# Optimization experiments

Measured on AMD Instinct MI355X. Metric: run time of the kernel, lower is better.

The kernel has to match this reference:

```python
import jax, jax.numpy as jnp
import numpy as np

# shapes
B, S, D, V = 2, 2048, 1024, 32000
C = 8            # n_cycles
P = 256          # actual planes = min(n_planes_init, D // 2)
EPS = 1.1920929e-07  # torch RMSNorm default eps for float32 (finfo.eps)


def _rmsnorm(x, w):
    ms = jnp.mean(x * x, axis=-1, keepdims=True)
    return x * jax.lax.rsqrt(ms + EPS) * w


def setup_inputs() -> dict:
    key = jax.random.key(0)
    ks = jax.random.split(key, 10)
    tokens = jax.random.randint(ks[0], (B, S), 0, V, dtype=jnp.int32)
    embed_weight = jax.random.normal(ks[1], (V, D), dtype=jnp.float32) * 0.02
    lm_head_weight = jax.random.normal(ks[2], (V, D), dtype=jnp.float32) * 0.02
    out_norm_weight = jnp.ones((D,), dtype=jnp.float32)
    # per-cycle learned params (non-trivial values for numerics)
    angles = jax.random.normal(ks[3], (C, P), dtype=jnp.float32) * 0.1
    scales = 1.0 + jax.random.normal(ks[4], (C, D), dtype=jnp.float32) * 0.01
    shifts = jax.random.normal(ks[5], (C, D), dtype=jnp.float32) * 0.01
    norm_weights = 1.0 + jax.random.normal(ks[6], (C, D), dtype=jnp.float32) * 0.01
    mix_weight = jnp.array([0.1, 0.8, 0.1], dtype=jnp.float32)
    # plane pairs: per-cycle permutation of D, pi = perm[:P], pj = perm[P:2P]
    pi_list, pj_list = [], []
    for c in range(C):
        perm = jax.random.permutation(jax.random.fold_in(ks[7], c), D)
        pi_list.append(perm[:P])
        pj_list.append(perm[P:2 * P])
    pi_all = jnp.stack(pi_list).astype(jnp.int32)  # [C, P]
    pj_all = jnp.stack(pj_list).astype(jnp.int32)  # [C, P]
    return {
        "tokens": tokens,
        "embed_weight": embed_weight,
        "angles": angles,
        "scales": scales,
        "shifts": shifts,
        "norm_weights": norm_weights,
        "mix_weight": mix_weight,
        "out_norm_weight": out_norm_weight,
        "lm_head_weight": lm_head_weight,
        "pi_all": pi_all,
        "pj_all": pj_all,
    }


def reference(tokens, embed_weight, angles, scales, shifts, norm_weights,
              mix_weight, out_norm_weight, lm_head_weight, pi_all, pj_all):
    x = embed_weight[tokens].astype(jnp.float32)  # [B, S, D]
    n_cycles = angles.shape[0]
    for c in range(n_cycles):
        # temporal mix: shifted-left / self / shifted-right
        left = jnp.pad(x[:, :-1, :], ((0, 0), (1, 0), (0, 0)))
        right = jnp.pad(x[:, 1:, :], ((0, 0), (0, 1), (0, 0)))
        x = mix_weight[0] * left + mix_weight[1] * x + mix_weight[2] * right
        # Givens rotations on disjoint plane pairs (gather -> rotate -> scatter)
        pi, pj = pi_all[c], pj_all[c]
        cos_a = jnp.cos(angles[c])
        sin_a = jnp.sin(angles[c])
        xi = x[..., pi]  # [B, S, P]
        xj = x[..., pj]
        x_new = x.at[..., pi].set(xi * cos_a - xj * sin_a)
        x_new = x_new.at[..., pj].set(xi * sin_a + xj * cos_a)
        # scale/shift + SiLU, then RMSNorm residual update
        x_act = jax.nn.silu(x_new * scales[c] + shifts[c])
        x = x + _rmsnorm(x_act - x, norm_weights[c])
    x = _rmsnorm(x, out_norm_weight)
    return jnp.einsum("bsd,vd->bsv", x, lm_head_weight)  # [B, S, V]
```

## Files before the change

kernel.cpp:

```cpp
#include <hip/hip_runtime.h>

#define B_SZ   2
#define S_LEN  2048
#define D_DIM  1024
#define V_DIM  32000
#define NTOK   (B_SZ * S_LEN)
#define NCYC   8
#define NPLANES 256
#define EPS_F  1.1920929e-07f
#define NTILE  2000

typedef float  f32x4  __attribute__((ext_vector_type(4)));
typedef __bf16 bf16x8 __attribute__((ext_vector_type(8)));

__device__ __forceinline__ unsigned short f32_to_bf16(float f) {
    unsigned int u = __builtin_bit_cast(unsigned int, f);
    u += 0x7fffu + ((u >> 16) & 1u);
    return (unsigned short)(u >> 16);
}

__global__ __launch_bounds__(512, 2) void k_chain(
    const int* __restrict__ tokens, const float* __restrict__ table,
    const float* __restrict__ angles, const float* __restrict__ scales,
    const float* __restrict__ shifts, const float* __restrict__ normw,
    const float* __restrict__ mixw, const float* __restrict__ outnw,
    const int* __restrict__ pi_all, const int* __restrict__ pj_all,
    const float* __restrict__ lmhead,
    unsigned short* __restrict__ xbf, unsigned short* __restrict__ wbf)
{
    __shared__ float lx[32][D_DIM];
    __shared__ float red[8][32];
    const int blk = blockIdx.x, tid = threadIdx.x;
    const int wv = tid >> 6, ln = tid & 63;
    const int t0 = blk << 4;
    const int s0 = t0 & (S_LEN - 1);
    const int seqbase = t0 & ~(S_LEN - 1);
    const int c2 = tid << 1;

    const float mw0 = mixw[0], mw1 = mixw[1], mw2 = mixw[2];

    unsigned int svmask = 0;
    #pragma unroll
    for (int r = 0; r < 32; ++r) {
        const int s = s0 - 8 + r;
        const bool sv = (s >= 0) && (s < S_LEN);
        if (sv) svmask |= (1u << r);
        float2 v = make_float2(0.f, 0.f);
        if (sv) {
            const int tok = tokens[seqbase + s];
            v = *(const float2*)(table + (size_t)tok * D_DIM + c2);
        }
        lx[r][c2] = v.x; lx[r][c2 + 1] = v.y;
    }
    __syncthreads();

    float2 mreg[31], rres[31];

    for (int c = 0; c < NCYC; ++c) {
        const float2 sc = *(const float2*)(scales + c * D_DIM + c2);
        const float2 sh = *(const float2*)(shifts + c * D_DIM + c2);
        const float2 nw = *(const float2*)(normw  + c * D_DIM + c2);
        const int p    = tid & 255;
        const int half = tid >> 8;
        const int ip = pi_all[c * NPLANES + p];
        const int jp = pj_all[c * NPLANES + p];
        float sa, ca;
        sincosf(angles[c * NPLANES + p], &sa, &ca);

        #pragma unroll
        for (int r = 1; r <= 30; ++r) {
            if (r >= c + 1 && r < 31 - c && ((svmask >> r) & 1)) {
                const float2 a = make_float2(lx[r - 1][c2], lx[r - 1][c2 + 1]);
                const float2 b = make_float2(lx[r][c2],     lx[r][c2 + 1]);
                const float2 d = make_float2(lx[r + 1][c2], lx[r + 1][c2 + 1]);
                mreg[r].x = mw0 * a.x + mw1 * b.x + mw2 * d.x;
                mreg[r].y = mw0 * a.y + mw1 * b.y + mw2 * d.y;
            }
        }
        __syncthreads();
        #pragma unroll
        for (int r = 1; r <= 30; ++r) {
            if (r >= c + 1 && r < 31 - c && ((svmask >> r) & 1)) {
                lx[r][c2] = mreg[r].x; lx[r][c2 + 1] = mreg[r].y;
            }
        }
        __syncthreads();
        #pragma unroll
        for (int r = 1; r <= 30; ++r) {
            if (r >= c + 1 && r < 31 - c && ((svmask >> r) & 1) && (r & 1) == half) {
                const float xi = lx[r][ip], xj = lx[r][jp];
                lx[r][ip] = xi * ca - xj * sa;
                lx[r][jp] = xi * sa + xj * ca;
            }
        }
        __syncthreads();
        #pragma unroll
        for (int r = 1; r <= 30; ++r) {
            if (r >= c + 1 && r < 31 - c && ((svmask >> r) & 1)) {
                const float v0 = lx[r][c2], v1 = lx[r][c2 + 1];
                const float a0 = v0 * sc.x + sh.x;
                const float a1 = v1 * sc.y + sh.y;
                rres[r].x = a0 / (1.f + expf(-a0)) - mreg[r].x;
                rres[r].y = a1 / (1.f + expf(-a1)) - mreg[r].y;
                float pp = rres[r].x * rres[r].x + rres[r].y * rres[r].y;
                #pragma unroll
                for (int off = 32; off > 0; off >>= 1)
                    pp += __shfl_down(pp, off, 64);
                if (ln == 0) red[wv][r] = pp;
            }
        }
        __syncthreads();
        #pragma unroll
        for (int r = 1; r <= 30; ++r) {
            if (r >= c + 1 && r < 31 - c && ((svmask >> r) & 1)) {
                const float tot = red[0][r] + red[1][r] + red[2][r] + red[3][r]
                                + red[4][r] + red[5][r] + red[6][r] + red[7][r];
                const float inv = rsqrtf(tot * (1.0f / D_DIM) + EPS_F);
                lx[r][c2]     = mreg[r].x + rres[r].x * inv * nw.x;
                lx[r][c2 + 1] = mreg[r].y + rres[r].y * inv * nw.y;
            }
        }
        __syncthreads();
    }

    const float2 ow = *(const float2*)(outnw + c2);
    #pragma unroll
    for (int r = 8; r < 24; ++r) {
        const float v0 = lx[r][c2], v1 = lx[r][c2 + 1];
        float pp = v0 * v0 + v1 * v1;
        #pragma unroll
        for (int off = 32; off > 0; off >>= 1)
            pp += __shfl_down(pp, off, 64);
        if (ln == 0) red[wv][r - 8] = pp;
    }
    __syncthreads();
    #pragma unroll
    for (int r = 8; r < 24; ++r) {
        const float tot = red[0][r - 8] + red[1][r - 8] + red[2][r - 8] + red[3][r - 8]
                        + red[4][r - 8] + red[5][r - 8] + red[6][r - 8] + red[7][r - 8];
        const float inv = rsqrtf(tot * (1.0f / D_DIM) + EPS_F);
        const float v0 = lx[r][c2], v1 = lx[r][c2 + 1];
        ushort2 o = make_ushort2(f32_to_bf16(v0 * inv * ow.x),
                                 f32_to_bf16(v1 * inv * ow.y));
        *(ushort2*)(xbf + (size_t)(t0 + r - 8) * D_DIM + c2) = o;
    }

    for (int i = blk * 512 + tid; i < (V_DIM * D_DIM) / 4; i += 256 * 512) {
        const float4 v = ((const float4*)lmhead)[i];
        const ushort4 o = make_ushort4(f32_to_bf16(v.x), f32_to_bf16(v.y),
                                       f32_to_bf16(v.z), f32_to_bf16(v.w));
        ((ushort4*)wbf)[i] = o;
    }
}

#define GLD_LDS(g, l)                                                          \
    __builtin_amdgcn_global_load_lds(                                          \
        (const __attribute__((address_space(1))) void*)(g),                    \
        (__attribute__((address_space(3))) void*)(l), 16, 0, 0)

#define STAGE_A(BUF, H, KT, P) do {                                            \
    GLD_LDS((P) + (size_t)(H) * 131072 + (size_t)(KT) * 64,                    \
            &lds[(BUF) * 32768 + (H) * 8192 + wave * 1024]);                   \
    GLD_LDS((P) + (size_t)(H) * 131072 + 8192 + (size_t)(KT) * 64,             \
            &lds[(BUF) * 32768 + (H) * 8192 + wave * 1024 + 512]);             \
} while (0)

#define STAGE_B(BUF, H, KT, P) do {                                            \
    GLD_LDS((P) + (size_t)(H) * 131072 + (size_t)(KT) * 64,                    \
            &lds[16384 + (BUF) * 32768 + (H) * 8192 + wave * 1024]);           \
    GLD_LDS((P) + (size_t)(H) * 131072 + 8192 + (size_t)(KT) * 64,             \
            &lds[16384 + (BUF) * 32768 + (H) * 8192 + wave * 1024 + 512]);     \
} while (0)

#define RD_A(BUF, MIB) do { _Pragma("unroll")                                  \
    for (int q_ = 0; q_ < 4; ++q_) {                                           \
        afr[q_][0] = *(const bf16x8*)&lds[(BUF) * 32768 + aoff + ((MIB) + q_) * 1024 + kx0]; \
        afr[q_][1] = *(const bf16x8*)&lds[(BUF) * 32768 + aoff + ((MIB) + q_) * 1024 + kx1]; \
    } } while (0)

#define RD_B(BUF, NIB, DST) do { _Pragma("unroll")                             \
    for (int n_ = 0; n_ < 2; ++n_) {                                           \
        DST[n_][0] = *(const bf16x8*)&lds[(BUF) * 32768 + boff + ((NIB) + n_) * 1024 + kx0]; \
        DST[n_][1] = *(const bf16x8*)&lds[(BUF) * 32768 + boff + ((NIB) + n_) * 1024 + kx1]; \
    } } while (0)

#define MFMA16(MIB, NIB, BF) do {                                              \
    __builtin_amdgcn_s_setprio(1);                                             \
    _Pragma("unroll") for (int m_ = 0; m_ < 4; ++m_)                           \
    _Pragma("unroll") for (int n_ = 0; n_ < 2; ++n_) {                         \
        acc[(MIB) + m_][(NIB) + n_] = __builtin_amdgcn_mfma_f32_16x16x32_bf16( \
            afr[m_][0], BF[n_][0], acc[(MIB) + m_][(NIB) + n_], 0, 0, 0);      \
        acc[(MIB) + m_][(NIB) + n_] = __builtin_amdgcn_mfma_f32_16x16x32_bf16( \
            afr[m_][1], BF[n_][1], acc[(MIB) + m_][(NIB) + n_], 0, 0, 0);      \
    }                                                                          \
    __builtin_amdgcn_s_setprio(0); } while (0)

#define PH_SYNC() do { __builtin_amdgcn_s_barrier();                           \
    asm volatile("s_waitcnt lgkmcnt(0)" ::: "memory"); } while (0)
#define PH_END() do { asm volatile("" ::: "memory");                           \
    __builtin_amdgcn_s_barrier(); } while (0)
#define VMCNT4() asm volatile("s_waitcnt vmcnt(4)" ::: "memory")

__global__ __launch_bounds__(512, 2) void k_gemm(
    const unsigned short* __restrict__ A,
    const unsigned short* __restrict__ Bw,
    float* __restrict__ C)
{
    __shared__ __align__(16) unsigned short lds[65536];
    const int tid = threadIdx.x;
    const int wave = tid >> 6, lane = tid & 63;
    const int wm = wave >> 2, wn = wave & 3;
    const int lr = lane & 15, kg = lane >> 4;

    const int xr  = (lane & 7) * 8;
    const int kx0 = (kg * 8) ^ xr;
    const int kx1 = (32 + kg * 8) ^ xr;
    const int aoff = (wm * 128 + lr) * 64;
    const int boff = 16384 + (wn * 64 + lr) * 64;

    const int srow = lane >> 3;
    const int scol = ((lane & 7) ^ srow) * 8;
    const int soff = (wave * 16 + srow) * 1024 + scol;

    const int xcd = blockIdx.x & 7;
    const int rr  = blockIdx.x >> 3;
    const int tbase = xcd * 250 + rr * 8;
    const int ntile_mine = (rr == 31) ? 2 : 8;

    int T  = tbase;
    int bm = T & 15, bn = T >> 4;
    const unsigned short* gA = A  + (size_t)(bm * 256) * 1024 + soff;
    const unsigned short* gB = Bw + (size_t)(bn * 256) * 1024 + soff;

    bf16x8 afr[4][2], b01[2][2], b23[2][2];

    STAGE_A(0, 0, 0, gA); STAGE_A(0, 1, 0, gA);
    STAGE_B(0, 0, 0, gB); STAGE_B(0, 1, 0, gB);
    STAGE_B(1, 0, 1, gB); STAGE_B(1, 1, 1, gB);
    VMCNT4();
    __builtin_amdgcn_s_barrier();

    for (int t = 0; t < ntile_mine; ++t) {
        const bool last = (t == ntile_mine - 1);
        const int Tn = last ? T : T + 1;
        const int bm2 = Tn & 15, bn2 = Tn >> 4;
        const unsigned short* gA2 = A  + (size_t)(bm2 * 256) * 1024 + soff;
        const unsigned short* gB2 = Bw + (size_t)(bn2 * 256) * 1024 + soff;

        f32x4 acc[8][4];
        #pragma unroll
        for (int i = 0; i < 8; ++i)
            #pragma unroll
            for (int j2 = 0; j2 < 4; ++j2) acc[i][j2] = (f32x4){0.f, 0.f, 0.f, 0.f};

        for (int j = 0; j < 8; ++j) {
            const unsigned short* sA = (j == 7) ? gA2 : gA;
            const unsigned short* sB = (j == 7) ? gB2 : gB;
            const int k1 = 2 * j + 1;
            const int k2 = (2 * j + 2) & 15;
            const int k3 = (2 * j + 3) & 15;

            RD_A(0, 0); RD_B(0, 0, b01);
            STAGE_A(1, 0, k1, gA);
            PH_SYNC(); MFMA16(0, 0, b01); PH_END();

            RD_B(0, 2, b23);
            STAGE_A(1, 1, k1, gA);
            PH_SYNC(); MFMA16(0, 2, b23); PH_END();

            RD_A(0, 4);
            STAGE_B(0, 0, k2, sB);
            PH_SYNC(); MFMA16(4, 2, b23); PH_END();

            STAGE_B(0, 1, k2, sB);
            VMCNT4();
            PH_SYNC(); MFMA16(4, 0, b01); PH_END();

            RD_A(1, 0); RD_B(1, 0, b01);
            STAGE_A(0, 0, k2, sA);
            PH_SYNC(); MFMA16(0, 0, b01); PH_END();

            RD_B(1, 2, b23);
            STAGE_A(0, 1, k2, sA);
            PH_SYNC(); MFMA16(0, 2, b23); PH_END();

            RD_A(1, 4);
            STAGE_B(1, 0, k3, sB);
            PH_SYNC(); MFMA16(4, 2, b23); PH_END();

            STAGE_B(1, 1, k3, sB);
            VMCNT4();
            PH_SYNC(); MFMA16(4, 0, b01); PH_END();
        }

        #pragma unroll
        for (int mi = 0; mi < 8; ++mi) {
            const size_t m0 = (size_t)(bm * 256 + wm * 128 + mi * 16 + kg * 4);
            #pragma unroll
            for (int ni = 0; ni < 4; ++ni) {
                const int n = bn * 256 + wn * 64 + ni * 16 + lr;
                float* cp = C + m0 * V_DIM + n;
                cp[0]                 = acc[mi][ni][0];
                cp[(size_t)V_DIM]     = acc[mi][ni][1];
                cp[(size_t)2 * V_DIM] = acc[mi][ni][2];
                cp[(size_t)3 * V_DIM] = acc[mi][ni][3];
            }
        }

        T = Tn; bm = bm2; bn = bn2; gA = gA2; gB = gB2;
    }
}

extern "C" void kernel_launch(void* const* d_in, const int* in_sizes, int n_in,
                              void* d_out, int out_size, void* d_ws, size_t ws_size,
                              hipStream_t stream)
{
    const int*   tokens = (const int*)  d_in[0];
    const float* embedw = (const float*)d_in[1];
    const float* angles = (const float*)d_in[2];
    const float* scales = (const float*)d_in[3];
    const float* shifts = (const float*)d_in[4];
    const float* normw  = (const float*)d_in[5];
    const float* mixw   = (const float*)d_in[6];
    const float* outnw  = (const float*)d_in[7];
    const float* lmhead = (const float*)d_in[8];
    const int*   pi_all = (const int*)  d_in[9];
    const int*   pj_all = (const int*)  d_in[10];
    float* out = (float*)d_out;

    unsigned short* xbf = (unsigned short*)d_ws;
    unsigned short* wbf = xbf + (size_t)NTOK * D_DIM;

    k_chain<<<NTOK / 16, 512, 0, stream>>>(tokens, embedw, angles, scales,
        shifts, normw, mixw, outnw, pi_all, pj_all, lmhead, xbf, wbf);

    k_gemm<<<256, 512, 0, stream>>>(xbf, wbf, out);
}
```

Measured before the change: 467.9 us.

## Assign rows to waves in chain kernel and interleave weight conversion per cycle

```diff
diff --git a/kernel.cpp b/kernel.cpp
--- a/kernel.cpp
+++ b/kernel.cpp
@@ -29,127 +29,170 @@
     unsigned short* __restrict__ xbf, unsigned short* __restrict__ wbf)
 {
     __shared__ float lx[32][D_DIM];
-    __shared__ float red[8][32];
     const int blk = blockIdx.x, tid = threadIdx.x;
     const int wv = tid >> 6, ln = tid & 63;
     const int t0 = blk << 4;
     const int s0 = t0 & (S_LEN - 1);
     const int seqbase = t0 & ~(S_LEN - 1);
-    const int c2 = tid << 1;
+    const int r0 = wv << 2;
 
     const float mw0 = mixw[0], mw1 = mixw[1], mw2 = mixw[2];
 
-    unsigned int svmask = 0;
+    bool valid[4];
     #pragma unroll
-    for (int r = 0; r < 32; ++r) {
+    for (int i = 0; i < 4; ++i) {
+        const int r = r0 + i;
         const int s = s0 - 8 + r;
-        const bool sv = (s >= 0) && (s < S_LEN);
-        if (sv) svmask |= (1u << r);
-        float2 v = make_float2(0.f, 0.f);
-        if (sv) {
-            const int tok = tokens[seqbase + s];
-            v = *(const float2*)(table + (size_t)tok * D_DIM + c2);
-        }
-        lx[r][c2] = v.x; lx[r][c2 + 1] = v.y;
+        valid[i] = (s >= 0) && (s < S_LEN);
+        float4 v0 = make_float4(0.f,0.f,0.f,0.f), v1 = v0, v2 = v0, v3 = v0;
+        if (valid[i]) {
+            const float* tr = table + (size_t)tokens[seqbase + s] * D_DIM;
+            v0 = *(const float4*)(tr +   0 + ln * 4);
+            v1 = *(const float4*)(tr + 256 + ln * 4);
+            v2 = *(const float4*)(tr + 512 + ln * 4);
+            v3 = *(const float4*)(tr + 768 + ln * 4);
+        }
+        *(float4*)&lx[r][  0 + ln * 4] = v0;
+        *(float4*)&lx[r][256 + ln * 4] = v1;
+        *(float4*)&lx[r][512 + ln * 4] = v2;
+        *(float4*)&lx[r][768 + ln * 4] = v3;
     }
     __syncthreads();
 
-    float2 mreg[31], rres[31];
+    float4 mreg[4][4];
 
     for (int c = 0; c < NCYC; ++c) {
-        const float2 sc = *(const float2*)(scales + c * D_DIM + c2);
-        const float2 sh = *(const float2*)(shifts + c * D_DIM + c2);
-        const float2 nw = *(const float2*)(normw  + c * D_DIM + c2);
-        const int p    = tid & 255;
-        const int half = tid >> 8;
-        const int ip = pi_all[c * NPLANES + p];
-        const int jp = pj_all[c * NPLANES + p];
-        float sa, ca;
-        sincosf(angles[c * NPLANES + p], &sa, &ca);
-
-        #pragma unroll
-        for (int r = 1; r <= 30; ++r) {
-            if (r >= c + 1 && r < 31 - c && ((svmask >> r) & 1)) {
-                const float2 a = make_float2(lx[r - 1][c2], lx[r - 1][c2 + 1]);
-                const float2 b = make_float2(lx[r][c2],     lx[r][c2 + 1]);
-                const float2 d = make_float2(lx[r + 1][c2], lx[r + 1][c2 + 1]);
-                mreg[r].x = mw0 * a.x + mw1 * b.x + mw2 * d.x;
-                mreg[r].y = mw0 * a.y + mw1 * b.y + mw2 * d.y;
+        float4 sc[4], sh[4], nw[4];
+        #pragma unroll
+        for (int q = 0; q < 4; ++q) {
+            sc[q] = *(const float4*)(scales + c * D_DIM + q * 256 + ln * 4);
+            sh[q] = *(const float4*)(shifts + c * D_DIM + q * 256 + ln * 4);
+            nw[q] = *(const float4*)(normw  + c * D_DIM + q * 256 + ln * 4);
+        }
+        int ip[4], jp[4];
+        float sa[4], ca[4];
+        #pragma unroll
+        for (int u = 0; u < 4; ++u) {
+            ip[u] = pi_all[c * NPLANES + ln * 4 + u];
+            jp[u] = pj_all[c * NPLANES + ln * 4 + u];
+            sincosf(angles[c * NPLANES + ln * 4 + u], &sa[u], &ca[u]);
+        }
+
+        #pragma unroll
+        for (int i = 0; i < 4; ++i) {
+            const int r = r0 + i;
+            if (r >= c + 1 && r < 31 - c && valid[i]) {
+                #pragma unroll
+                for (int q = 0; q < 4; ++q) {
+                    const float4 a = *(const float4*)&lx[r - 1][q * 256 + ln * 4];
+                    const float4 b = *(const float4*)&lx[r    ][q * 256 + ln * 4];
+                    const float4 d = *(const float4*)&lx[r + 1][q * 256 + ln * 4];
+                    mreg[i][q].x = mw0 * a.x + mw1 * b.x + mw2 * d.x;
+                    mreg[i][q].y = mw0 * a.y + mw1 * b.y + mw2 * d.y;
+                    mreg[i][q].z = mw0 * a.z + mw1 * b.z + mw2 * d.z;
+                    mreg[i][q].w = mw0 * a.w + mw1 * b.w + mw2 * d.w;
+                }
             }
         }
         __syncthreads();
         #pragma unroll
-        for (int r = 1; r <= 30; ++r) {
-            if (r >= c + 1 && r < 31 - c && ((svmask >> r) & 1)) {
-                lx[r][c2] = mreg[r].x; lx[r][c2 + 1] = mreg[r].y;
-            }
-        }
-        __syncthreads();
-        #pragma unroll
-        for (int r = 1; r <= 30; ++r) {
-            if (r >= c + 1 && r < 31 - c && ((svmask >> r) & 1) && (r & 1) == half) {
-                const float xi = lx[r][ip], xj = lx[r][jp];
-                lx[r][ip] = xi * ca - xj * sa;
-                lx[r][jp] = xi * sa + xj * ca;
-            }
-        }
-        __syncthreads();
-        #pragma unroll
-        for (int r = 1; r <= 30; ++r) {
-            if (r >= c + 1 && r < 31 - c && ((svmask >> r) & 1)) {
-                const float v0 = lx[r][c2], v1 = lx[r][c2 + 1];
-                const float a0 = v0 * sc.x + sh.x;
-                const float a1 = v1 * sc.y + sh.y;
-                rres[r].x = a0 / (1.f + expf(-a0)) - mreg[r].x;
-                rres[r].y = a1 / (1.f + expf(-a1)) - mreg[r].y;
-                float pp = rres[r].x * rres[r].x + rres[r].y * rres[r].y;
+        for (int i = 0; i < 4; ++i) {
+            const int r = r0 + i;
+            if (r >= c + 1 && r < 31 - c && valid[i]) {
+                #pragma unroll
+                for (int q = 0; q < 4; ++q)
+                    *(float4*)&lx[r][q * 256 + ln * 4] = mreg[i][q];
+            }
+        }
+        #pragma unroll
+        for (int i = 0; i < 4; ++i) {
+            const int r = r0 + i;
+            if (r >= c + 1 && r < 31 - c && valid[i]) {
+                float xi[4], xj[4];
+                #pragma unroll
+                for (int u = 0; u < 4; ++u) { xi[u] = lx[r][ip[u]]; xj[u] = lx[r][jp[u]]; }
+                #pragma unroll
+                for (int u = 0; u < 4; ++u) {
+                    lx[r][ip[u]] = xi[u] * ca[u] - xj[u] * sa[u];
+                    lx[r][jp[u]] = xi[u] * sa[u] + xj[u] * ca[u];
+                }
+            }
+        }
+        #pragma unroll
+        for (int i = 0; i < 4; ++i) {
+            const int r = r0 + i;
+            if (r >= c + 1 && r < 31 - c && valid[i]) {
+                float4 rr[4];
+                float sum = 0.f;
+                #pragma unroll
+                for (int q = 0; q < 4; ++q) {
+                    const float4 xn = *(const float4*)&lx[r][q * 256 + ln * 4];
+                    const float a0 = xn.x * sc[q].x + sh[q].x;
+                    const float a1 = xn.y * sc[q].y + sh[q].y;
+                    const float a2 = xn.z * sc[q].z + sh[q].z;
+                    const float a3 = xn.w * sc[q].w + sh[q].w;
+                    rr[q].x = a0 / (1.f + expf(-a0)) - mreg[i][q].x;
+                    rr[q].y = a1 / (1.f + expf(-a1)) - mreg[i][q].y;
+                    rr[q].z = a2 / (1.f + expf(-a2)) - mreg[i][q].z;
+                    rr[q].w = a3 / (1.f + expf(-a3)) - mreg[i][q].w;
+                    sum += rr[q].x * rr[q].x + rr[q].y * rr[q].y
+                         + rr[q].z * rr[q].z + rr[q].w * rr[q].w;
+                }
                 #pragma unroll
                 for (int off = 32; off > 0; off >>= 1)
-                    pp += __shfl_down(pp, off, 64);
-                if (ln == 0) red[wv][r] = pp;
-            }
-        }
-        __syncthreads();
-        #pragma unroll
-        for (int r = 1; r <= 30; ++r) {
-            if (r >= c + 1 && r < 31 - c && ((svmask >> r) & 1)) {
-                const float tot = red[0][r] + red[1][r] + red[2][r] + red[3][r]
-                                + red[4][r] + red[5][r] + red[6][r] + red[7][r];
-                const float inv = rsqrtf(tot * (1.0f / D_DIM) + EPS_F);
-                lx[r][c2]     = mreg[r].x + rres[r].x * inv * nw.x;
-                lx[r][c2 + 1] = mreg[r].y + rres[r].y * inv * nw.y;
+                    sum += __shfl_xor(sum, off, 64);
+                const float inv = rsqrtf(sum * (1.0f / D_DIM) + EPS_F);
+                #pragma unroll
+                for (int q = 0; q < 4; ++q) {
+                    float4 o;
+                    o.x = mreg[i][q].x + rr[q].x * inv * nw[q].x;
+                    o.y = mreg[i][q].y + rr[q].y * inv * nw[q].y;
+                    o.z = mreg[i][q].z + rr[q].z * inv * nw[q].z;
+                    o.w = mreg[i][q].w + rr[q].w * inv * nw[q].w;
+                    *(float4*)&lx[r][q * 256 + ln * 4] = o;
+                }
+            }
+        }
+        {
+            const int end = (c + 1) * 1024000;
+            for (int idx = c * 1024000 + blk * 512 + tid; idx < end; idx += 131072) {
+                const float4 v = ((const float4*)lmhead)[idx];
+                const ushort4 o = make_ushort4(f32_to_bf16(v.x), f32_to_bf16(v.y),
+                                               f32_to_bf16(v.z), f32_to_bf16(v.w));
+                ((ushort4*)wbf)[idx] = o;
             }
         }
         __syncthreads();
     }
 
-    const float2 ow = *(const float2*)(outnw + c2);
+    float4 ow[4];
     #pragma unroll
-    for (int r = 8; r < 24; ++r) {
-        const float v0 = lx[r][c2], v1 = lx[r][c2 + 1];
-        float pp = v0 * v0 + v1 * v1;
+    for (int q = 0; q < 4; ++q)
+        ow[q] = *(const float4*)(outnw + q * 256 + ln * 4);
+    #pragma unroll
+    for (int e = 0; e < 2; ++e) {
+        const int r = 8 + wv + e * 8;
+        float4 v[4];
+        float sum = 0.f;
+        #pragma unroll
+        for (int q = 0; q < 4; ++q) {
+            v[q] = *(const float4*)&lx[r][q * 256 + ln * 4];
+            sum += v[q].x * v[q].x + v[q].y * v[q].y
+                 + v[q].z * v[q].z + v[q].w * v[q].w;
+        }
         #pragma unroll
         for (int off = 32; off > 0; off >>= 1)
-            pp += __shfl_down(pp, off, 64);
-        if (ln == 0) red[wv][r - 8] = pp;
-    }
-    __syncthreads();
-    #pragma unroll
-    for (int r = 8; r < 24; ++r) {
-        const float tot = red[0][r - 8] + red[1][r - 8] + red[2][r - 8] + red[3][r - 8]
-                        + red[4][r - 8] + red[5][r - 8] + red[6][r - 8] + red[7][r - 8];
-        const float inv = rsqrtf(tot * (1.0f / D_DIM) + EPS_F);
-        const float v0 = lx[r][c2], v1 = lx[r][c2 + 1];
-        ushort2 o = make_ushort2(f32_to_bf16(v0 * inv * ow.x),
-                                 f32_to_bf16(v1 * inv * ow.y));
-        *(ushort2*)(xbf + (size_t)(t0 + r - 8) * D_DIM + c2) = o;
-    }
-
-    for (int i = blk * 512 + tid; i < (V_DIM * D_DIM) / 4; i += 256 * 512) {
-        const float4 v = ((const float4*)lmhead)[i];
-        const ushort4 o = make_ushort4(f32_to_bf16(v.x), f32_to_bf16(v.y),
-                                       f32_to_bf16(v.z), f32_to_bf16(v.w));
-        ((ushort4*)wbf)[i] = o;
+            sum += __shfl_xor(sum, off, 64);
+        const float inv = rsqrtf(sum * (1.0f / D_DIM) + EPS_F);
+        unsigned short* xr = xbf + (size_t)(t0 + r - 8) * D_DIM;
+        #pragma unroll
+        for (int q = 0; q < 4; ++q) {
+            const ushort4 o = make_ushort4(f32_to_bf16(v[q].x * inv * ow[q].x),
+                                           f32_to_bf16(v[q].y * inv * ow[q].y),
+                                           f32_to_bf16(v[q].z * inv * ow[q].z),
+                                           f32_to_bf16(v[q].w * inv * ow[q].w));
+            *(ushort4*)(xr + q * 256 + ln * 4) = o;
+        }
     }
 }
 
```

Measured after the change: 410.9 us. 12.2% less time.
